# Kernel tuning notes

Hardware: AMD Instinct MI355X
Metric: run time of the kernel (lower is better)

Reference implementation:

```python
import jax, jax.numpy as jnp
import numpy as np

H = 30          # num attention heads
KVH = 6         # num key/value heads
D = 64          # head dim
HID = 1920      # hidden size
THETA = 10000.0
WINDOW = 1024   # sliding window size
EPS = 1e-5


def setup_inputs() -> dict:
    key = jax.random.key(0)
    ks = jax.random.split(key, 8)
    B, S = 1, 2048
    scale = 0.02
    return {
        "hidden_states": jax.random.normal(ks[0], (B, S, HID), jnp.float32),
        "position_ids": jnp.arange(S, dtype=jnp.int64)[None, :],
        "Wq": jax.random.normal(ks[1], (H * D, HID), jnp.float32) * scale,
        "Wk": jax.random.normal(ks[2], (KVH * D, HID), jnp.float32) * scale,
        "Wv": jax.random.normal(ks[3], (KVH * D, HID), jnp.float32) * scale,
        "Wo": jax.random.normal(ks[4], (HID, H * D), jnp.float32) * scale,
        "q_ln_w": jnp.ones((H, D), jnp.float32) + 0.01 * jax.random.normal(ks[5], (H, D)),
        "k_ln_w": jnp.ones((KVH, D), jnp.float32) + 0.01 * jax.random.normal(ks[6], (KVH, D)),
        "q_alpha": jnp.ones((1,), jnp.float32),
        "k_alpha": jnp.ones((1,), jnp.float32),
        "v_alpha": jnp.ones((1,), jnp.float32),
        "o_alpha": jnp.ones((1,), jnp.float32),
    }


def _rotate_half(x):
    h = x.shape[-1] // 2
    return jnp.concatenate([-x[..., h:], x[..., :h]], axis=-1)


def _per_head_layernorm(x, w):
    # x: [B, nh, S, D]; w: [nh, D]; LayerNorm over D, no bias (biased variance as torch)
    mu = x.mean(-1, keepdims=True)
    var = jnp.mean((x - mu) ** 2, axis=-1, keepdims=True)
    return (x - mu) * jax.lax.rsqrt(var + EPS) * w[None, :, None, :]


def _rope_tables(seq_len):
    inv_freq = 1.0 / (THETA ** (jnp.arange(0, D, 2, dtype=jnp.float32) / D))
    t = jnp.arange(seq_len, dtype=jnp.float32)
    freqs = jnp.outer(t, inv_freq)                      # [S, D/2]
    emb = jnp.concatenate([freqs, freqs], axis=-1)      # [S, D]
    return jnp.cos(emb), jnp.sin(emb)


def reference(hidden_states, position_ids, Wq, Wk, Wv, Wo,
              q_ln_w, k_ln_w, q_alpha, k_alpha, v_alpha, o_alpha):
    B, S, _ = hidden_states.shape

    q = (hidden_states @ Wq.T) * q_alpha    # [B,S,H*D]
    k = (hidden_states @ Wk.T) * k_alpha    # [B,S,KVH*D]
    v = (hidden_states @ Wv.T) * v_alpha

    q = q.reshape(B, S, H, D).transpose(0, 2, 1, 3)      # [B,H,S,D]
    k = k.reshape(B, S, KVH, D).transpose(0, 2, 1, 3)    # [B,KVH,S,D]
    v = v.reshape(B, S, KVH, D).transpose(0, 2, 1, 3)

    # per-head LayerNorm on Q/K
    q = _per_head_layernorm(q, q_ln_w)
    k = _per_head_layernorm(k, k_ln_w)

    # RoPE in fp32, cos/sin gathered by position_ids and unsqueezed on head dim
    cos, sin = _rope_tables(S)                            # [S, D]
    cos = cos[position_ids][:, None, :, :]                # [B,1,S,D]
    sin = sin[position_ids][:, None, :, :]
    q = q.astype(jnp.float32) * cos + _rotate_half(q.astype(jnp.float32)) * sin
    k = k.astype(jnp.float32) * cos + _rotate_half(k.astype(jnp.float32)) * sin

    # GQA: repeat kv heads
    n_rep = H // KVH
    k = jnp.repeat(k, n_rep, axis=1)                      # [B,H,S,D]
    v = jnp.repeat(v, n_rep, axis=1)

    scores = jnp.einsum("bhqd,bhkd->bhqk", q, k) / jnp.sqrt(jnp.float32(D))

    # sliding-window causal mask: attend to j <= i and i - j < WINDOW
    i = jnp.arange(S)[:, None]
    j = jnp.arange(S)[None, :]
    mask = (j <= i) & ((i - j) < WINDOW)                  # [S,S]
    neg = jnp.finfo(jnp.float32).min
    scores = jnp.where(mask[None, None], scores, neg)

    attn = jax.nn.softmax(scores.astype(jnp.float32), axis=-1).astype(v.dtype)
    out = jnp.einsum("bhqk,bhkd->bhqd", attn, v)          # [B,H,S,D]
    out = out.transpose(0, 2, 1, 3).reshape(B, S, H * D)
    out = (out @ Wo.T) * o_alpha                          # [B,S,HID]
    return out
```

## Files before the change

kernel.cpp:

```cpp
#include <hip/hip_runtime.h>
#include <hip/hip_fp16.h>

#define SS 2048
#define HH 30
#define KVHH 6
#define DD 64
#define HIDD 1920
#define NQKV 2688

typedef __attribute__((ext_vector_type(4))) float  f32x4;
typedef __attribute__((ext_vector_type(4))) float  float4v;
typedef __attribute__((ext_vector_type(8))) _Float16 f16x8;
typedef __attribute__((ext_vector_type(4))) _Float16 f16x4;

__global__ __launch_bounds__(256) void cvt_all(const float* __restrict__ hs,
                                               const float* __restrict__ Wq,
                                               const float* __restrict__ Wk,
                                               const float* __restrict__ Wv,
                                               const float* __restrict__ Wo,
                                               _Float16* __restrict__ hsb,
                                               _Float16* __restrict__ wqkvb,
                                               _Float16* __restrict__ wob,
                                               const float* __restrict__ qa,
                                               const float* __restrict__ ka,
                                               const float* __restrict__ va,
                                               const float* __restrict__ oa) {
    int b = blockIdx.x;
    const float* in; _Float16* out; float a; int base;
    if (b < 3840)      { in = hs; out = hsb;              a = 1.0f;  base = b; }
    else if (b < 7440) { in = Wq; out = wqkvb;            a = qa[0]; base = b - 3840; }
    else if (b < 8160) { in = Wk; out = wqkvb + 3686400;  a = ka[0]; base = b - 7440; }
    else if (b < 8880) { in = Wv; out = wqkvb + 4423680;  a = va[0]; base = b - 8160; }
    else               { in = Wo; out = wob;              a = oa[0]; base = b - 8880; }
    int i = base * 1024 + threadIdx.x * 4;
    float4v v = *(const float4v*)(in + i);
    f16x4 o;
    o[0] = (_Float16)(v[0] * a);
    o[1] = (_Float16)(v[1] * a);
    o[2] = (_Float16)(v[2] * a);
    o[3] = (_Float16)(v[3] * a);
    *(f16x4*)(out + i) = o;
}

#define GEMM_STAGE(buf, ktv)                                                                           \
    do {                                                                                               \
        _Pragma("unroll")                                                                              \
        for (int it = 0; it < 4; ++it) {                                                               \
            int gg  = it * 256 + tid;                                                                  \
            int row = gg >> 3;                                                                         \
            int sl  = (gg & 7) ^ (row & 7);                                                            \
            const _Float16* gA = A + (size_t)(m0 + row) * K + (ktv) + sl * 8;                          \
            const _Float16* gB = B + (size_t)(n0 + row) * K + (ktv) + sl * 8;                          \
            _Float16* lA = As[buf] + (size_t)(it * 256 + w * 64) * 8;                                  \
            _Float16* lB = Bs[buf] + (size_t)(it * 256 + w * 64) * 8;                                  \
            __builtin_amdgcn_global_load_lds((const __attribute__((address_space(1))) unsigned int*)gA,\
                                             (__attribute__((address_space(3))) unsigned int*)lA, 16, 0, 0); \
            __builtin_amdgcn_global_load_lds((const __attribute__((address_space(1))) unsigned int*)gB,\
                                             (__attribute__((address_space(3))) unsigned int*)lB, 16, 0, 0); \
        }                                                                                              \
    } while (0)

__global__ __launch_bounds__(256) void gemm_bt_f16(const _Float16* __restrict__ A,
                                                   const _Float16* __restrict__ B,
                                                   float* __restrict__ C,
                                                   int M, int N, int K) {
    __shared__ __align__(16) _Float16 As[2][128 * 64];
    __shared__ __align__(16) _Float16 Bs[2][128 * 64];
    const int tid = threadIdx.x;
    const int l   = tid & 63;
    const int w   = tid >> 6;
    const int wm  = (w >> 1) * 64;
    const int wn  = (w & 1) * 64;

    const int gx  = gridDim.x;
    const int nwg = gx * gridDim.y;
    int bid = blockIdx.y * gx + blockIdx.x;
    int lid = (bid & 7) * (nwg >> 3) + (bid >> 3);
    int by  = lid / gx;
    int bx  = lid - by * gx;

    const int m0 = by * 128;
    const int n0 = bx * 128;

    f32x4 acc[4][4];
#pragma unroll
    for (int a = 0; a < 4; ++a)
#pragma unroll
        for (int b = 0; b < 4; ++b) acc[a][b] = (f32x4)0.0f;

    GEMM_STAGE(0, 0);
    __syncthreads();

    const int nk = K >> 6;
    for (int t = 0; t < nk; ++t) {
        const int cur = t & 1;
        if (t + 1 < nk) GEMM_STAGE(cur ^ 1, (t + 1) * 64);

#pragma unroll
        for (int kk = 0; kk < 2; ++kk) {
            f16x8 af[4], bf[4];
#pragma unroll
            for (int fm = 0; fm < 4; ++fm) {
                int row = wm + fm * 16 + (l & 15);
                int s   = (kk * 4 + (l >> 4)) ^ (row & 7);
                af[fm] = *(const f16x8*)(As[cur] + row * 64 + s * 8);
            }
#pragma unroll
            for (int fn = 0; fn < 4; ++fn) {
                int row = wn + fn * 16 + (l & 15);
                int s   = (kk * 4 + (l >> 4)) ^ (row & 7);
                bf[fn] = *(const f16x8*)(Bs[cur] + row * 64 + s * 8);
            }
#pragma unroll
            for (int fm = 0; fm < 4; ++fm)
#pragma unroll
                for (int fn = 0; fn < 4; ++fn)
                    acc[fm][fn] = __builtin_amdgcn_mfma_f32_16x16x32_f16(af[fm], bf[fn], acc[fm][fn], 0, 0, 0);
        }
        __syncthreads();
    }

#pragma unroll
    for (int fm = 0; fm < 4; ++fm)
#pragma unroll
        for (int fn = 0; fn < 4; ++fn)
#pragma unroll
            for (int j = 0; j < 4; ++j) {
                int r = m0 + wm + fm * 16 + (l >> 4) * 4 + j;
                int c = n0 + wn + fn * 16 + (l & 15);
                C[(size_t)r * N + c] = acc[fm][fn][j];
            }
}

__global__ __launch_bounds__(256) void lnrope(const float* __restrict__ qkv,
                                              const float* __restrict__ qlnw,
                                              const float* __restrict__ klnw,
                                              _Float16* __restrict__ Qh,
                                              _Float16* __restrict__ Kh,
                                              _Float16* __restrict__ Vh) {
    int task = blockIdx.x * 4 + (threadIdx.x >> 6);
    int lane = threadIdx.x & 63;
    int s = task / 42;
    int u = task % 42;
    if (s >= SS) return;

    if (u < 36) {
        int head  = (u < 30) ? u : (u - 30);
        int col   = (u < 30) ? (u * 64 + lane) : (1920 + head * 64 + lane);
        const float* lw = (u < 30) ? qlnw : klnw;
        float x = qkv[(size_t)s * NQKV + col];

        float mu = x;
#pragma unroll
        for (int off = 32; off; off >>= 1) mu += __shfl_xor(mu, off);
        mu *= (1.0f / 64.0f);
        float d = x - mu;
        float var = d * d;
#pragma unroll
        for (int off = 32; off; off >>= 1) var += __shfl_xor(var, off);
        var *= (1.0f / 64.0f);
        float xn = d * rsqrtf(var + 1e-5f) * lw[head * 64 + lane];

        float f = exp2f(-13.287712379549449f * (float)(lane & 31) * (1.0f / 32.0f));
        float ang = (float)s * f;
        float sn, cs;
        sincosf(ang, &sn, &cs);
        float prt = __shfl_xor(xn, 32);
        float rot = (lane < 32) ? -prt : prt;
        float r = xn * cs + rot * sn;

        if (u < 30) Qh[((size_t)head * SS + s) * 64 + lane] = (_Float16)(r * 0.125f);
        else        Kh[((size_t)head * SS + s) * 64 + lane] = (_Float16)r;
    } else {
        int head = u - 36;
        float x = qkv[(size_t)s * NQKV + 2304 + head * 64 + lane];
        Vh[((size_t)head * SS + s) * 64 + lane] = (_Float16)x;
    }
}

__global__ __launch_bounds__(256) void transpose_v(const _Float16* __restrict__ Vh,
                                                   _Float16* __restrict__ Vt) {
    __shared__ _Float16 T[64][68];
    const int s0 = blockIdx.x * 64;
    const int h  = blockIdx.y;
    const int tid = threadIdx.x;
#pragma unroll
    for (int pass = 0; pass < 2; ++pass) {
        int idx = pass * 256 + tid;
        int r = idx >> 3, d0 = (idx & 7) * 8;
        f16x8 v = *(const f16x8*)(Vh + ((size_t)(h * SS + s0 + r)) * 64 + d0);
#pragma unroll
        for (int j = 0; j < 8; ++j) T[r][d0 + j] = v[j];
    }
    __syncthreads();
#pragma unroll
    for (int pass = 0; pass < 2; ++pass) {
        int idx = pass * 256 + tid;
        int d = idx >> 3, c0 = (idx & 7) * 8;
        f16x8 o;
#pragma unroll
        for (int j = 0; j < 8; ++j) o[j] = T[c0 + j][d];
        *(f16x8*)(Vt + ((size_t)(h * 64 + d)) * SS + s0 + c0) = o;
    }
}

#define ATTN_STAGE(buf, c)                                                                             \
    do {                                                                                               \
        _Pragma("unroll")                                                                              \
        for (int t = 0; t < 2; ++t) {                                                                  \
            int rloc = w * 16 + t * 8 + (l >> 3);                                                      \
            int ss = (l & 7) ^ (l >> 3);                                                               \
            const _Float16* gK = Kh + ((size_t)kvh * SS + (c) * 64 + rloc) * 64 + ss * 8;              \
            const _Float16* gV = Vt + ((size_t)kvh * 64 + rloc) * SS + (c) * 64 + ss * 8;              \
            _Float16* lK = Ks[buf] + (w * 16 + t * 8) * 64;                                            \
            _Float16* lV = Vs[buf] + (w * 16 + t * 8) * 64;                                            \
            __builtin_amdgcn_global_load_lds((const __attribute__((address_space(1))) unsigned int*)gK,\
                                             (__attribute__((address_space(3))) unsigned int*)lK, 16, 0, 0); \
            __builtin_amdgcn_global_load_lds((const __attribute__((address_space(1))) unsigned int*)gV,\
                                             (__attribute__((address_space(3))) unsigned int*)lV, 16, 0, 0); \
        }                                                                                              \
    } while (0)

__global__ __launch_bounds__(256) void attn_mfma(const _Float16* __restrict__ Qh,
                                                 const _Float16* __restrict__ Kh,
                                                 const _Float16* __restrict__ Vt,
                                                 _Float16* __restrict__ Ob) {
    __shared__ __align__(16) _Float16 Ks[2][64 * 64];
    __shared__ __align__(16) _Float16 Vs[2][64 * 64];
    __shared__ __align__(16) _Float16 Ps[4][16 * 64];

    const int qb = 31 - blockIdx.x;
    const int h = blockIdx.y;
    const int Q0 = qb * 64;
    const int kvh = h / 5;
    const int tid = threadIdx.x, l = tid & 63, w = tid >> 6;
    const int g = l >> 4, li = l & 15;
    const int qabs = Q0 + w * 16 + li;

    f16x8 qf[2];
#pragma unroll
    for (int dk = 0; dk < 2; ++dk)
        qf[dk] = *(const f16x8*)(Qh + ((size_t)h * SS + qabs) * 64 + dk * 32 + g * 8);

    float m_i = -1e20f, l_i = 0.0f;
    f32x4 o[4];
#pragma unroll
    for (int fn = 0; fn < 4; ++fn) o[fn] = (f32x4)0.0f;

    const int c_lo = (Q0 >= 1023) ? ((Q0 - 1023) >> 6) : 0;
    const int c_hi = qb;
    const int qw = Q0 + w * 16;

    ATTN_STAGE(0, c_lo);
    __syncthreads();

    for (int c = c_lo; c <= c_hi; ++c) {
        const int nb = (c - c_lo) & 1;
        if (c < c_hi) ATTN_STAGE(nb ^ 1, c + 1);

        if (c * 64 <= qw + 15 && c * 64 + 63 >= qw - 1023) {
            const _Float16* Kb = Ks[nb];
            const _Float16* Vb = Vs[nb];
            const bool full = (c * 64 + 63 <= qw) && (c * 64 >= qw + 15 - 1023);

            f32x4 st[4];
#pragma unroll
            for (int f = 0; f < 4; ++f) st[f] = (f32x4)0.0f;
            __builtin_amdgcn_s_setprio(1);
#pragma unroll
            for (int dk = 0; dk < 2; ++dk) {
#pragma unroll
                for (int f = 0; f < 4; ++f) {
                    int ps = (dk * 4 + g) ^ (li & 7);
                    f16x8 kf = *(const f16x8*)(Kb + (f * 16 + li) * 64 + ps * 8);
                    st[f] = __builtin_amdgcn_mfma_f32_16x16x32_f16(kf, qf[dk], st[f], 0, 0, 0);
                }
            }
            __builtin_amdgcn_s_setprio(0);

            if (!full) {
#pragma unroll
                for (int f = 0; f < 4; ++f)
#pragma unroll
                    for (int reg = 0; reg < 4; ++reg) {
                        int kab = c * 64 + f * 16 + g * 4 + reg;
                        bool valid = (kab <= qabs) && (qabs - kab < 1024);
                        st[f][reg] = valid ? st[f][reg] : -1e30f;
                    }
            }
            float mx = -1e30f;
#pragma unroll
            for (int f = 0; f < 4; ++f)
#pragma unroll
                for (int reg = 0; reg < 4; ++reg) mx = fmaxf(mx, st[f][reg]);
            mx = fmaxf(mx, __shfl_xor(mx, 16));
            mx = fmaxf(mx, __shfl_xor(mx, 32));

            if (__any(mx > m_i + 6.0f)) {
                float m_new = fmaxf(m_i, mx);
                float corr = __expf(m_i - m_new);
                m_i = m_new;
                l_i *= corr;
                float c0 = __shfl(corr, g * 4 + 0);
                float c1 = __shfl(corr, g * 4 + 1);
                float c2 = __shfl(corr, g * 4 + 2);
                float c3 = __shfl(corr, g * 4 + 3);
#pragma unroll
                for (int fn = 0; fn < 4; ++fn) {
                    o[fn][0] *= c0; o[fn][1] *= c1; o[fn][2] *= c2; o[fn][3] *= c3;
                }
            }

            float psum = 0.0f;
            char* Pw = (char*)&Ps[w][0] + li * 128;
#pragma unroll
            for (int f = 0; f < 4; ++f)
#pragma unroll
                for (int rp = 0; rp < 2; ++rp) {
                    float p0 = __expf(st[f][2 * rp]     - m_i);
                    float p1 = __expf(st[f][2 * rp + 1] - m_i);
                    psum += p0 + p1;
                    union { _Float16 hh[2]; unsigned u; } pk;
                    pk.hh[0] = (_Float16)p0; pk.hh[1] = (_Float16)p1;
                    int phys = (f * 2 + (g >> 1)) ^ (li & 7);
                    *(unsigned*)(Pw + phys * 16 + (g & 1) * 8 + rp * 4) = pk.u;
                }
            psum += __shfl_xor(psum, 16);
            psum += __shfl_xor(psum, 32);
            l_i += psum;

            __builtin_amdgcn_s_setprio(1);
#pragma unroll
            for (int kk = 0; kk < 2; ++kk) {
                int pp = (kk * 4 + g) ^ (li & 7);
                f16x8 pa = *(const f16x8*)(Pw + pp * 16);
#pragma unroll
                for (int fn = 0; fn < 4; ++fn) {
                    int drow = fn * 16 + li;
                    int vp = (kk * 4 + g) ^ (li & 7);
                    f16x8 vf = *(const f16x8*)(Vb + drow * 64 + vp * 8);
                    o[fn] = __builtin_amdgcn_mfma_f32_16x16x32_f16(pa, vf, o[fn], 0, 0, 0);
                }
            }
            __builtin_amdgcn_s_setprio(0);
        }
        __syncthreads();
    }

#pragma unroll
    for (int reg = 0; reg < 4; ++reg) {
        float linv = 1.0f / __shfl(l_i, g * 4 + reg);
        int row = Q0 + w * 16 + g * 4 + reg;
#pragma unroll
        for (int fn = 0; fn < 4; ++fn)
            Ob[(size_t)row * HIDD + h * 64 + fn * 16 + li] = (_Float16)(o[fn][reg] * linv);
    }
}

extern "C" void kernel_launch(void* const* d_in, const int* in_sizes, int n_in,
                              void* d_out, int out_size, void* d_ws, size_t ws_size,
                              hipStream_t stream) {
    const float* hs   = (const float*)d_in[0];
    const float* Wq   = (const float*)d_in[2];
    const float* Wk   = (const float*)d_in[3];
    const float* Wv   = (const float*)d_in[4];
    const float* Wo   = (const float*)d_in[5];
    const float* qlnw = (const float*)d_in[6];
    const float* klnw = (const float*)d_in[7];
    const float* qa   = (const float*)d_in[8];
    const float* ka   = (const float*)d_in[9];
    const float* va   = (const float*)d_in[10];
    const float* oa   = (const float*)d_in[11];

    char* ws = (char*)d_ws;
    _Float16* hsb   = (_Float16*)ws;                 ws += (size_t)SS * HIDD * 2;
    _Float16* wqkvb = (_Float16*)ws;                 ws += (size_t)NQKV * HIDD * 2;
    _Float16* wob   = (_Float16*)ws;                 ws += (size_t)HIDD * HIDD * 2;
    float*    qkv   = (float*)ws;                    ws += (size_t)SS * NQKV * 4;
    _Float16* Qhd   = (_Float16*)ws;                 ws += (size_t)HH * SS * DD * 2;
    _Float16* Khd   = (_Float16*)ws;                 ws += (size_t)KVHH * SS * DD * 2;
    _Float16* Vhd   = (_Float16*)ws;                 ws += (size_t)KVHH * SS * DD * 2;
    _Float16* Vtd   = (_Float16*)ws;                 ws += (size_t)KVHH * SS * DD * 2;
    _Float16* attnb = (_Float16*)ws;                 ws += (size_t)SS * HIDD * 2;

    cvt_all<<<12480, 256, 0, stream>>>(hs, Wq, Wk, Wv, Wo, hsb, wqkvb, wob, qa, ka, va, oa);

    gemm_bt_f16<<<dim3(NQKV / 128, SS / 128), 256, 0, stream>>>(hsb, wqkvb, qkv, SS, NQKV, HIDD);

    lnrope<<<(SS * 42) / 4, 256, 0, stream>>>(qkv, qlnw, klnw, Qhd, Khd, Vhd);

    transpose_v<<<dim3(SS / 64, KVHH), 256, 0, stream>>>(Vhd, Vtd);

    attn_mfma<<<dim3(SS / 64, HH), 256, 0, stream>>>(Qhd, Khd, Vtd, attnb);

    gemm_bt_f16<<<dim3(HIDD / 128, SS / 128), 256, 0, stream>>>(attnb, wob, (float*)d_out, SS, HIDD, HIDD);
}
```

Measured before the change: 146.4 us.

## Double query tile per attention block with triple-buffered KV and exp2 softmax

The attention kernel now gives each block 128 query rows instead of 64, with each wave handling two 16-row fragments. Every K/V tile loaded into LDS is therefore reused by twice as many queries, and the grid is halved. The LDS ring goes from two to three buffers, using explicit vmcnt waits and one barrier per iteration instead of two __syncthreads. log2(e) is folded into the Q scale so the softmax can use exp2f, and the rescale threshold is raised. The cost is more registers per wave, fewer blocks (which may hurt occupancy and load balance), and the per-wave skipping of fully masked chunks is dropped.

Measured after the change: 155.4 us. +6.1%, slower.

```diff
diff --git a/kernel.cpp b/kernel.cpp
--- a/kernel.cpp
+++ b/kernel.cpp
@@ -169,7 +169,7 @@
         float rot = (lane < 32) ? -prt : prt;
         float r = xn * cs + rot * sn;
 
-        if (u < 30) Qh[((size_t)head * SS + s) * 64 + lane] = (_Float16)(r * 0.125f);
+        if (u < 30) Qh[((size_t)head * SS + s) * 64 + lane] = (_Float16)(r * 0.18033688011112042f);
         else        Kh[((size_t)head * SS + s) * 64 + lane] = (_Float16)r;
     } else {
         int head = u - 36;
@@ -212,8 +212,8 @@
             int ss = (l & 7) ^ (l >> 3);                                                               \
             const _Float16* gK = Kh + ((size_t)kvh * SS + (c) * 64 + rloc) * 64 + ss * 8;              \
             const _Float16* gV = Vt + ((size_t)kvh * 64 + rloc) * SS + (c) * 64 + ss * 8;              \
-            _Float16* lK = Ks[buf] + (w * 16 + t * 8) * 64;                                            \
-            _Float16* lV = Vs[buf] + (w * 16 + t * 8) * 64;                                            \
+            _Float16* lK = KsB + (buf) * 4096 + (w * 16 + t * 8) * 64;                                 \
+            _Float16* lV = VsB + (buf) * 4096 + (w * 16 + t * 8) * 64;                                 \
             __builtin_amdgcn_global_load_lds((const __attribute__((address_space(1))) unsigned int*)gK,\
                                              (__attribute__((address_space(3))) unsigned int*)lK, 16, 0, 0); \
             __builtin_amdgcn_global_load_lds((const __attribute__((address_space(1))) unsigned int*)gV,\
@@ -225,100 +225,121 @@
                                                  const _Float16* __restrict__ Kh,
                                                  const _Float16* __restrict__ Vt,
                                                  _Float16* __restrict__ Ob) {
-    __shared__ __align__(16) _Float16 Ks[2][64 * 64];
-    __shared__ __align__(16) _Float16 Vs[2][64 * 64];
-    __shared__ __align__(16) _Float16 Ps[4][16 * 64];
-
-    const int qb = 31 - blockIdx.x;
+    __shared__ __align__(16) _Float16 smem[32768];
+    _Float16* const KsB = smem;
+    _Float16* const VsB = smem + 12288;
+    _Float16* const PsB = smem + 24576;
+
+    const int qb = 15 - blockIdx.x;
     const int h = blockIdx.y;
-    const int Q0 = qb * 64;
+    const int Q0 = qb * 128;
     const int kvh = h / 5;
     const int tid = threadIdx.x, l = tid & 63, w = tid >> 6;
     const int g = l >> 4, li = l & 15;
-    const int qabs = Q0 + w * 16 + li;
-
-    f16x8 qf[2];
-#pragma unroll
-    for (int dk = 0; dk < 2; ++dk)
-        qf[dk] = *(const f16x8*)(Qh + ((size_t)h * SS + qabs) * 64 + dk * 32 + g * 8);
-
-    float m_i = -1e20f, l_i = 0.0f;
-    f32x4 o[4];
-#pragma unroll
-    for (int fn = 0; fn < 4; ++fn) o[fn] = (f32x4)0.0f;
+    const int qw = Q0 + w * 32;
+
+    f16x8 qf[2][2];
+#pragma unroll
+    for (int fr = 0; fr < 2; ++fr)
+#pragma unroll
+        for (int dk = 0; dk < 2; ++dk)
+            qf[fr][dk] = *(const f16x8*)(Qh + ((size_t)h * SS + qw + fr * 16 + li) * 64 + dk * 32 + g * 8);
+    asm volatile("s_waitcnt vmcnt(0)" ::: "memory");
+
+    float m_i[2] = {-1e20f, -1e20f}, l_i[2] = {0.0f, 0.0f};
+    f32x4 o[2][4];
+#pragma unroll
+    for (int fr = 0; fr < 2; ++fr)
+#pragma unroll
+        for (int fn = 0; fn < 4; ++fn) o[fr][fn] = (f32x4)0.0f;
 
     const int c_lo = (Q0 >= 1023) ? ((Q0 - 1023) >> 6) : 0;
-    const int c_hi = qb;
-    const int qw = Q0 + w * 16;
+    const int c_hi = qb * 2 + 1;
 
     ATTN_STAGE(0, c_lo);
-    __syncthreads();
-
+
+    int cur = 0, nxt = 1;
     for (int c = c_lo; c <= c_hi; ++c) {
-        const int nb = (c - c_lo) & 1;
-        if (c < c_hi) ATTN_STAGE(nb ^ 1, c + 1);
-
-        if (c * 64 <= qw + 15 && c * 64 + 63 >= qw - 1023) {
-            const _Float16* Kb = Ks[nb];
-            const _Float16* Vb = Vs[nb];
-            const bool full = (c * 64 + 63 <= qw) && (c * 64 >= qw + 15 - 1023);
-
-            f32x4 st[4];
-#pragma unroll
-            for (int f = 0; f < 4; ++f) st[f] = (f32x4)0.0f;
-            __builtin_amdgcn_s_setprio(1);
-#pragma unroll
-            for (int dk = 0; dk < 2; ++dk) {
-#pragma unroll
-                for (int f = 0; f < 4; ++f) {
-                    int ps = (dk * 4 + g) ^ (li & 7);
-                    f16x8 kf = *(const f16x8*)(Kb + (f * 16 + li) * 64 + ps * 8);
-                    st[f] = __builtin_amdgcn_mfma_f32_16x16x32_f16(kf, qf[dk], st[f], 0, 0, 0);
-                }
-            }
-            __builtin_amdgcn_s_setprio(0);
-
-            if (!full) {
+        if (c + 1 <= c_hi) {
+            ATTN_STAGE(nxt, c + 1);
+            asm volatile("s_waitcnt vmcnt(4)" ::: "memory");
+        } else {
+            asm volatile("s_waitcnt vmcnt(0)" ::: "memory");
+        }
+        __builtin_amdgcn_s_barrier();
+        __builtin_amdgcn_sched_barrier(0);
+
+        const _Float16* Kb = KsB + cur * 4096;
+        const _Float16* Vb = VsB + cur * 4096;
+
+        f32x4 st[2][4];
+#pragma unroll
+        for (int fr = 0; fr < 2; ++fr)
+#pragma unroll
+            for (int f = 0; f < 4; ++f) st[fr][f] = (f32x4)0.0f;
+
+        __builtin_amdgcn_s_setprio(1);
+#pragma unroll
+        for (int dk = 0; dk < 2; ++dk) {
+#pragma unroll
+            for (int f = 0; f < 4; ++f) {
+                int ps = (dk * 4 + g) ^ (li & 7);
+                f16x8 kf = *(const f16x8*)(Kb + (f * 16 + li) * 64 + ps * 8);
+                st[0][f] = __builtin_amdgcn_mfma_f32_16x16x32_f16(kf, qf[0][dk], st[0][f], 0, 0, 0);
+                st[1][f] = __builtin_amdgcn_mfma_f32_16x16x32_f16(kf, qf[1][dk], st[1][f], 0, 0, 0);
+            }
+        }
+        __builtin_amdgcn_s_setprio(0);
+
+        const bool full = (c * 64 + 63 <= qw) && (c * 64 >= qw + 31 - 1023);
+        if (!full) {
+#pragma unroll
+            for (int fr = 0; fr < 2; ++fr) {
+                int qa = qw + fr * 16 + li;
 #pragma unroll
                 for (int f = 0; f < 4; ++f)
 #pragma unroll
                     for (int reg = 0; reg < 4; ++reg) {
                         int kab = c * 64 + f * 16 + g * 4 + reg;
-                        bool valid = (kab <= qabs) && (qabs - kab < 1024);
-                        st[f][reg] = valid ? st[f][reg] : -1e30f;
+                        bool valid = (kab <= qa) && (qa - kab < 1024);
+                        st[fr][f][reg] = valid ? st[fr][f][reg] : -1e30f;
                     }
             }
+        }
+
+#pragma unroll
+        for (int fr = 0; fr < 2; ++fr) {
             float mx = -1e30f;
 #pragma unroll
             for (int f = 0; f < 4; ++f)
 #pragma unroll
-                for (int reg = 0; reg < 4; ++reg) mx = fmaxf(mx, st[f][reg]);
+                for (int reg = 0; reg < 4; ++reg) mx = fmaxf(mx, st[fr][f][reg]);
             mx = fmaxf(mx, __shfl_xor(mx, 16));
             mx = fmaxf(mx, __shfl_xor(mx, 32));
 
-            if (__any(mx > m_i + 6.0f)) {
-                float m_new = fmaxf(m_i, mx);
-                float corr = __expf(m_i - m_new);
-                m_i = m_new;
-                l_i *= corr;
+            if (__any(mx > m_i[fr] + 8.0f)) {
+                float m_new = fmaxf(m_i[fr], mx);
+                float corr = exp2f(m_i[fr] - m_new);
+                m_i[fr] = m_new;
+                l_i[fr] *= corr;
                 float c0 = __shfl(corr, g * 4 + 0);
                 float c1 = __shfl(corr, g * 4 + 1);
                 float c2 = __shfl(corr, g * 4 + 2);
                 float c3 = __shfl(corr, g * 4 + 3);
 #pragma unroll
                 for (int fn = 0; fn < 4; ++fn) {
-                    o[fn][0] *= c0; o[fn][1] *= c1; o[fn][2] *= c2; o[fn][3] *= c3;
+                    o[fr][fn][0] *= c0; o[fr][fn][1] *= c1; o[fr][fn][2] *= c2; o[fr][fn][3] *= c3;
                 }
             }
 
             float psum = 0.0f;
-            char* Pw = (char*)&Ps[w][0] + li * 128;
+            char* Pw = (char*)(PsB + w * 2048) + (fr * 16 + li) * 128;
 #pragma unroll
             for (int f = 0; f < 4; ++f)
 #pragma unroll
                 for (int rp = 0; rp < 2; ++rp) {
-                    float p0 = __expf(st[f][2 * rp]     - m_i);
-                    float p1 = __expf(st[f][2 * rp + 1] - m_i);
+                    float p0 = exp2f(st[fr][f][2 * rp]     - m_i[fr]);
+                    float p1 = exp2f(st[fr][f][2 * rp + 1] - m_i[fr]);
                     psum += p0 + p1;
                     union { _Float16 hh[2]; unsigned u; } pk;
                     pk.hh[0] = (_Float16)p0; pk.hh[1] = (_Float16)p1;
@@ -327,34 +348,40 @@
                 }
             psum += __shfl_xor(psum, 16);
             psum += __shfl_xor(psum, 32);
-            l_i += psum;
-
-            __builtin_amdgcn_s_setprio(1);
-#pragma unroll
-            for (int kk = 0; kk < 2; ++kk) {
-                int pp = (kk * 4 + g) ^ (li & 7);
-                f16x8 pa = *(const f16x8*)(Pw + pp * 16);
-#pragma unroll
-                for (int fn = 0; fn < 4; ++fn) {
-                    int drow = fn * 16 + li;
-                    int vp = (kk * 4 + g) ^ (li & 7);
-                    f16x8 vf = *(const f16x8*)(Vb + drow * 64 + vp * 8);
-                    o[fn] = __builtin_amdgcn_mfma_f32_16x16x32_f16(pa, vf, o[fn], 0, 0, 0);
-                }
-            }
-            __builtin_amdgcn_s_setprio(0);
-        }
-        __syncthreads();
+            l_i[fr] += psum;
+        }
+
+        char* PwB = (char*)(PsB + w * 2048);
+        __builtin_amdgcn_s_setprio(1);
+#pragma unroll
+        for (int kk = 0; kk < 2; ++kk) {
+            int pp = (kk * 4 + g) ^ (li & 7);
+            f16x8 pa0 = *(const f16x8*)(PwB + (li)      * 128 + pp * 16);
+            f16x8 pa1 = *(const f16x8*)(PwB + (16 + li) * 128 + pp * 16);
+#pragma unroll
+            for (int fn = 0; fn < 4; ++fn) {
+                int vp = (kk * 4 + g) ^ (li & 7);
+                f16x8 vf = *(const f16x8*)(Vb + (fn * 16 + li) * 64 + vp * 8);
+                o[0][fn] = __builtin_amdgcn_mfma_f32_16x16x32_f16(pa0, vf, o[0][fn], 0, 0, 0);
+                o[1][fn] = __builtin_amdgcn_mfma_f32_16x16x32_f16(pa1, vf, o[1][fn], 0, 0, 0);
+            }
+        }
+        __builtin_amdgcn_s_setprio(0);
+
+        cur = (cur == 2) ? 0 : cur + 1;
+        nxt = (nxt == 2) ? 0 : nxt + 1;
     }
 
 #pragma unroll
-    for (int reg = 0; reg < 4; ++reg) {
-        float linv = 1.0f / __shfl(l_i, g * 4 + reg);
-        int row = Q0 + w * 16 + g * 4 + reg;
-#pragma unroll
-        for (int fn = 0; fn < 4; ++fn)
-            Ob[(size_t)row * HIDD + h * 64 + fn * 16 + li] = (_Float16)(o[fn][reg] * linv);
-    }
+    for (int fr = 0; fr < 2; ++fr)
+#pragma unroll
+        for (int reg = 0; reg < 4; ++reg) {
+            float linv = 1.0f / __shfl(l_i[fr], g * 4 + reg);
+            int row = Q0 + w * 32 + fr * 16 + g * 4 + reg;
+#pragma unroll
+            for (int fn = 0; fn < 4; ++fn)
+                Ob[(size_t)row * HIDD + h * 64 + fn * 16 + li] = (_Float16)(o[fr][fn][reg] * linv);
+        }
 }
 
 extern "C" void kernel_launch(void* const* d_in, const int* in_sizes, int n_in,
@@ -391,7 +418,7 @@
 
     transpose_v<<<dim3(SS / 64, KVHH), 256, 0, stream>>>(Vhd, Vtd);
 
-    attn_mfma<<<dim3(SS / 64, HH), 256, 0, stream>>>(Qhd, Khd, Vtd, attnb);
+    attn_mfma<<<dim3(SS / 128, HH), 256, 0, stream>>>(Qhd, Khd, Vtd, attnb);
 
     gemm_bt_f16<<<dim3(HIDD / 128, SS / 128), 256, 0, stream>>>(attnb, wob, (float*)d_out, SS, HIDD, HIDD);
 }
```

## Use single-wave attention blocks reading K/V directly from global memory

Applied to the files above, without the earlier changes.

The attention kernel moves from 256-thread blocks that share double-buffered K/V tiles in LDS to one-wave blocks handling 16 query rows each, loading K and V fragments straight from global memory (relying on cache). This removes the LDS staging, block-wide barriers and the work wasted when warps in a block have different window ranges, and it makes the grid four times larger. It also folds log2(e) into the Q scale so exp2f replaces __expf, and raises the lazy-rescale threshold to 8 in log2 units. The cost is that K/V reuse across the query rows of a block is lost, so more global and L2 traffic, and the uncoalesced fragment loads may be slower.

Result: slower. 225.4 us (+54.0%).

```diff
diff --git a/kernel.cpp b/kernel.cpp
--- a/kernel.cpp
+++ b/kernel.cpp
@@ -169,7 +169,7 @@
         float rot = (lane < 32) ? -prt : prt;
         float r = xn * cs + rot * sn;
 
-        if (u < 30) Qh[((size_t)head * SS + s) * 64 + lane] = (_Float16)(r * 0.125f);
+        if (u < 30) Qh[((size_t)head * SS + s) * 64 + lane] = (_Float16)(r * 0.18033688011112042f);
         else        Kh[((size_t)head * SS + s) * 64 + lane] = (_Float16)r;
     } else {
         int head = u - 36;
@@ -204,38 +204,19 @@
     }
 }
 
-#define ATTN_STAGE(buf, c)                                                                             \
-    do {                                                                                               \
-        _Pragma("unroll")                                                                              \
-        for (int t = 0; t < 2; ++t) {                                                                  \
-            int rloc = w * 16 + t * 8 + (l >> 3);                                                      \
-            int ss = (l & 7) ^ (l >> 3);                                                               \
-            const _Float16* gK = Kh + ((size_t)kvh * SS + (c) * 64 + rloc) * 64 + ss * 8;              \
-            const _Float16* gV = Vt + ((size_t)kvh * 64 + rloc) * SS + (c) * 64 + ss * 8;              \
-            _Float16* lK = Ks[buf] + (w * 16 + t * 8) * 64;                                            \
-            _Float16* lV = Vs[buf] + (w * 16 + t * 8) * 64;                                            \
-            __builtin_amdgcn_global_load_lds((const __attribute__((address_space(1))) unsigned int*)gK,\
-                                             (__attribute__((address_space(3))) unsigned int*)lK, 16, 0, 0); \
-            __builtin_amdgcn_global_load_lds((const __attribute__((address_space(1))) unsigned int*)gV,\
-                                             (__attribute__((address_space(3))) unsigned int*)lV, 16, 0, 0); \
-        }                                                                                              \
-    } while (0)
-
-__global__ __launch_bounds__(256) void attn_mfma(const _Float16* __restrict__ Qh,
-                                                 const _Float16* __restrict__ Kh,
-                                                 const _Float16* __restrict__ Vt,
-                                                 _Float16* __restrict__ Ob) {
-    __shared__ __align__(16) _Float16 Ks[2][64 * 64];
-    __shared__ __align__(16) _Float16 Vs[2][64 * 64];
-    __shared__ __align__(16) _Float16 Ps[4][16 * 64];
-
-    const int qb = 31 - blockIdx.x;
-    const int h = blockIdx.y;
-    const int Q0 = qb * 64;
+__global__ __launch_bounds__(64) void attn_mfma(const _Float16* __restrict__ Qh,
+                                                const _Float16* __restrict__ Kh,
+                                                const _Float16* __restrict__ Vt,
+                                                _Float16* __restrict__ Ob) {
+    __shared__ __align__(16) _Float16 Ps[16 * 64];
+
+    const int qt = 127 - blockIdx.x;
+    const int h  = blockIdx.y;
+    const int qw = qt * 16;
     const int kvh = h / 5;
-    const int tid = threadIdx.x, l = tid & 63, w = tid >> 6;
+    const int l = threadIdx.x;
     const int g = l >> 4, li = l & 15;
-    const int qabs = Q0 + w * 16 + li;
+    const int qabs = qw + li;
 
     f16x8 qf[2];
 #pragma unroll
@@ -247,110 +228,97 @@
 #pragma unroll
     for (int fn = 0; fn < 4; ++fn) o[fn] = (f32x4)0.0f;
 
-    const int c_lo = (Q0 >= 1023) ? ((Q0 - 1023) >> 6) : 0;
-    const int c_hi = qb;
-    const int qw = Q0 + w * 16;
-
-    ATTN_STAGE(0, c_lo);
-    __syncthreads();
+    const int c_lo = (qw >= 1023) ? ((qw - 1023) >> 6) : 0;
+    const int c_hi = (qw + 15) >> 6;
 
     for (int c = c_lo; c <= c_hi; ++c) {
-        const int nb = (c - c_lo) & 1;
-        if (c < c_hi) ATTN_STAGE(nb ^ 1, c + 1);
-
-        if (c * 64 <= qw + 15 && c * 64 + 63 >= qw - 1023) {
-            const _Float16* Kb = Ks[nb];
-            const _Float16* Vb = Vs[nb];
-            const bool full = (c * 64 + 63 <= qw) && (c * 64 >= qw + 15 - 1023);
-
-            f32x4 st[4];
-#pragma unroll
-            for (int f = 0; f < 4; ++f) st[f] = (f32x4)0.0f;
-            __builtin_amdgcn_s_setprio(1);
-#pragma unroll
-            for (int dk = 0; dk < 2; ++dk) {
-#pragma unroll
-                for (int f = 0; f < 4; ++f) {
-                    int ps = (dk * 4 + g) ^ (li & 7);
-                    f16x8 kf = *(const f16x8*)(Kb + (f * 16 + li) * 64 + ps * 8);
-                    st[f] = __builtin_amdgcn_mfma_f32_16x16x32_f16(kf, qf[dk], st[f], 0, 0, 0);
+        const _Float16* Kc = Kh + ((size_t)kvh * SS + c * 64) * 64;
+        const _Float16* Vc = Vt + ((size_t)kvh * 64) * SS + c * 64;
+
+        f32x4 st[4];
+#pragma unroll
+        for (int f = 0; f < 4; ++f) st[f] = (f32x4)0.0f;
+        __builtin_amdgcn_s_setprio(1);
+#pragma unroll
+        for (int dk = 0; dk < 2; ++dk)
+#pragma unroll
+            for (int f = 0; f < 4; ++f) {
+                f16x8 kf = *(const f16x8*)(Kc + (f * 16 + li) * 64 + dk * 32 + g * 8);
+                st[f] = __builtin_amdgcn_mfma_f32_16x16x32_f16(kf, qf[dk], st[f], 0, 0, 0);
+            }
+        __builtin_amdgcn_s_setprio(0);
+
+        const bool full = (c * 64 + 63 <= qw) && (c * 64 >= qw + 15 - 1023);
+        if (!full) {
+#pragma unroll
+            for (int f = 0; f < 4; ++f)
+#pragma unroll
+                for (int reg = 0; reg < 4; ++reg) {
+                    int kab = c * 64 + f * 16 + g * 4 + reg;
+                    bool valid = (kab <= qabs) && (qabs - kab < 1024);
+                    st[f][reg] = valid ? st[f][reg] : -1e30f;
                 }
-            }
-            __builtin_amdgcn_s_setprio(0);
-
-            if (!full) {
-#pragma unroll
-                for (int f = 0; f < 4; ++f)
-#pragma unroll
-                    for (int reg = 0; reg < 4; ++reg) {
-                        int kab = c * 64 + f * 16 + g * 4 + reg;
-                        bool valid = (kab <= qabs) && (qabs - kab < 1024);
-                        st[f][reg] = valid ? st[f][reg] : -1e30f;
-                    }
-            }
-            float mx = -1e30f;
-#pragma unroll
-            for (int f = 0; f < 4; ++f)
-#pragma unroll
-                for (int reg = 0; reg < 4; ++reg) mx = fmaxf(mx, st[f][reg]);
-            mx = fmaxf(mx, __shfl_xor(mx, 16));
-            mx = fmaxf(mx, __shfl_xor(mx, 32));
-
-            if (__any(mx > m_i + 6.0f)) {
-                float m_new = fmaxf(m_i, mx);
-                float corr = __expf(m_i - m_new);
-                m_i = m_new;
-                l_i *= corr;
-                float c0 = __shfl(corr, g * 4 + 0);
-                float c1 = __shfl(corr, g * 4 + 1);
-                float c2 = __shfl(corr, g * 4 + 2);
-                float c3 = __shfl(corr, g * 4 + 3);
-#pragma unroll
-                for (int fn = 0; fn < 4; ++fn) {
-                    o[fn][0] *= c0; o[fn][1] *= c1; o[fn][2] *= c2; o[fn][3] *= c3;
-                }
-            }
-
-            float psum = 0.0f;
-            char* Pw = (char*)&Ps[w][0] + li * 128;
-#pragma unroll
-            for (int f = 0; f < 4; ++f)
-#pragma unroll
-                for (int rp = 0; rp < 2; ++rp) {
-                    float p0 = __expf(st[f][2 * rp]     - m_i);
-                    float p1 = __expf(st[f][2 * rp + 1] - m_i);
-                    psum += p0 + p1;
-                    union { _Float16 hh[2]; unsigned u; } pk;
-                    pk.hh[0] = (_Float16)p0; pk.hh[1] = (_Float16)p1;
-                    int phys = (f * 2 + (g >> 1)) ^ (li & 7);
-                    *(unsigned*)(Pw + phys * 16 + (g & 1) * 8 + rp * 4) = pk.u;
-                }
-            psum += __shfl_xor(psum, 16);
-            psum += __shfl_xor(psum, 32);
-            l_i += psum;
-
-            __builtin_amdgcn_s_setprio(1);
-#pragma unroll
-            for (int kk = 0; kk < 2; ++kk) {
-                int pp = (kk * 4 + g) ^ (li & 7);
-                f16x8 pa = *(const f16x8*)(Pw + pp * 16);
-#pragma unroll
-                for (int fn = 0; fn < 4; ++fn) {
-                    int drow = fn * 16 + li;
-                    int vp = (kk * 4 + g) ^ (li & 7);
-                    f16x8 vf = *(const f16x8*)(Vb + drow * 64 + vp * 8);
-                    o[fn] = __builtin_amdgcn_mfma_f32_16x16x32_f16(pa, vf, o[fn], 0, 0, 0);
-                }
-            }
-            __builtin_amdgcn_s_setprio(0);
         }
-        __syncthreads();
+
+        float mx = -1e30f;
+#pragma unroll
+        for (int f = 0; f < 4; ++f)
+#pragma unroll
+            for (int reg = 0; reg < 4; ++reg) mx = fmaxf(mx, st[f][reg]);
+        mx = fmaxf(mx, __shfl_xor(mx, 16));
+        mx = fmaxf(mx, __shfl_xor(mx, 32));
+
+        if (__any(mx > m_i + 8.0f)) {
+            float m_new = fmaxf(m_i, mx);
+            float corr = exp2f(m_i - m_new);
+            m_i = m_new;
+            l_i *= corr;
+            float c0 = __shfl(corr, g * 4 + 0);
+            float c1 = __shfl(corr, g * 4 + 1);
+            float c2 = __shfl(corr, g * 4 + 2);
+            float c3 = __shfl(corr, g * 4 + 3);
+#pragma unroll
+            for (int fn = 0; fn < 4; ++fn) {
+                o[fn][0] *= c0; o[fn][1] *= c1; o[fn][2] *= c2; o[fn][3] *= c3;
+            }
+        }
+
+        float psum = 0.0f;
+        char* Pw = (char*)Ps + li * 128;
+#pragma unroll
+        for (int f = 0; f < 4; ++f)
+#pragma unroll
+            for (int rp = 0; rp < 2; ++rp) {
+                float p0 = exp2f(st[f][2 * rp]     - m_i);
+                float p1 = exp2f(st[f][2 * rp + 1] - m_i);
+                psum += p0 + p1;
+                union { _Float16 hh[2]; unsigned u; } pk;
+                pk.hh[0] = (_Float16)p0; pk.hh[1] = (_Float16)p1;
+                int phys = (f * 2 + (g >> 1)) ^ (li & 7);
+                *(unsigned*)(Pw + phys * 16 + (g & 1) * 8 + rp * 4) = pk.u;
+            }
+        psum += __shfl_xor(psum, 16);
+        psum += __shfl_xor(psum, 32);
+        l_i += psum;
+
+        __builtin_amdgcn_s_setprio(1);
+#pragma unroll
+        for (int kk = 0; kk < 2; ++kk) {
+            int pp = (kk * 4 + g) ^ (li & 7);
+            f16x8 pa = *(const f16x8*)(Pw + pp * 16);
+#pragma unroll
+            for (int fn = 0; fn < 4; ++fn) {
+                f16x8 vf = *(const f16x8*)(Vc + (size_t)(fn * 16 + li) * SS + kk * 32 + g * 8);
+                o[fn] = __builtin_amdgcn_mfma_f32_16x16x32_f16(pa, vf, o[fn], 0, 0, 0);
+            }
+        }
+        __builtin_amdgcn_s_setprio(0);
     }
 
 #pragma unroll
     for (int reg = 0; reg < 4; ++reg) {
         float linv = 1.0f / __shfl(l_i, g * 4 + reg);
-        int row = Q0 + w * 16 + g * 4 + reg;
+        int row = qw + g * 4 + reg;
 #pragma unroll
         for (int fn = 0; fn < 4; ++fn)
             Ob[(size_t)row * HIDD + h * 64 + fn * 16 + li] = (_Float16)(o[fn][reg] * linv);
@@ -391,7 +359,7 @@
 
     transpose_v<<<dim3(SS / 64, KVHH), 256, 0, stream>>>(Vhd, Vtd);
 
-    attn_mfma<<<dim3(SS / 64, HH), 256, 0, stream>>>(Qhd, Khd, Vtd, attnb);
+    attn_mfma<<<dim3(SS / 16, HH), 64, 0, stream>>>(Qhd, Khd, Vtd, attnb);
 
     gemm_bt_f16<<<dim3(HIDD / 128, SS / 128), 256, 0, stream>>>(attnb, wob, (float*)d_out, SS, HIDD, HIDD);
 }
```
